# Optimization experiments

Hardware: AMD Instinct MI355X
Metric: run time of the kernel (lower is better)

The kernel has to match this reference:

```python
import jax, jax.numpy as jnp
import numpy as np

DIM = 4096
N_HEADS = 32
N_KV_HEADS = 8
HEAD_DIM = DIM // N_HEADS  # 128
SEQLEN = 2048
BATCH = 2
ROPE_THETA = 10000.0


def _precompute_freqs(seqlen, head_dim, theta):
    # matches torchtitan precompute_freqs_cis: freqs over even indices
    freqs = 1.0 / (theta ** (np.arange(0, head_dim, 2)[: head_dim // 2].astype(np.float32) / head_dim))
    t = np.arange(seqlen, dtype=np.float32)
    ang = np.outer(t, freqs)  # (S, head_dim//2)
    return jnp.asarray(np.cos(ang)), jnp.asarray(np.sin(ang))


def setup_inputs() -> dict:
    key = jax.random.key(0)
    kx, kq, kk, kv, ko = jax.random.split(key, 5)
    x = jax.random.normal(kx, (BATCH, SEQLEN, DIM), dtype=jnp.float32)
    wq = jax.random.normal(kq, (N_HEADS * HEAD_DIM, DIM), dtype=jnp.float32) * 0.02
    wk = jax.random.normal(kk, (N_KV_HEADS * HEAD_DIM, DIM), dtype=jnp.float32) * 0.02
    wv = jax.random.normal(kv, (N_KV_HEADS * HEAD_DIM, DIM), dtype=jnp.float32) * 0.02
    wo = jax.random.normal(ko, (DIM, N_HEADS * HEAD_DIM), dtype=jnp.float32) * 0.02
    cos, sin = _precompute_freqs(SEQLEN, HEAD_DIM, ROPE_THETA)
    return {"x": x, "cos": cos, "sin": sin, "wq": wq, "wk": wk, "wv": wv, "wo": wo}


def _apply_rope(t, cos, sin):
    # t: (B, S, H, hd); pairs (t[...,2i], t[...,2i+1]) rotated by angle
    tr = t.reshape(*t.shape[:-1], -1, 2)
    a, b = tr[..., 0], tr[..., 1]
    c = cos[None, :, None, :]  # (1, S, 1, hd//2)
    s = sin[None, :, None, :]
    out = jnp.stack([a * c - b * s, a * s + b * c], axis=-1)
    return out.reshape(t.shape)


def reference(x, cos, sin, wq, wk, wv, wo):
    B, S, D = x.shape
    hd = 2 * cos.shape[-1]
    H = wq.shape[0] // hd
    KVH = wk.shape[0] // hd
    n_rep = H // KVH

    q = (x @ wq.T).reshape(B, S, H, hd)
    k = (x @ wk.T).reshape(B, S, KVH, hd)
    v = (x @ wv.T).reshape(B, S, KVH, hd)

    q = _apply_rope(q, cos, sin)
    k = _apply_rope(k, cos, sin)

    # GQA: repeat_interleave kv heads (kept implicit via reshape of q into groups)
    qg = q.reshape(B, S, KVH, n_rep, hd)
    scale = 1.0 / jnp.sqrt(jnp.asarray(hd, dtype=x.dtype))
    # scores: (B, KVH, n_rep, S_q, S_k)
    scores = jnp.einsum("bsgrd,btgd->bgrst", qg, k) * scale
    causal = jnp.tril(jnp.ones((S, S), dtype=bool))
    scores = jnp.where(causal[None, None, None], scores, jnp.asarray(-1e30, dtype=scores.dtype))
    probs = jax.nn.softmax(scores, axis=-1)
    out = jnp.einsum("bgrst,btgd->bsgrd", probs, v).reshape(B, S, H * hd)
    return out @ wo.T
```

## Files before the change

### kernel.cpp

```cpp
#include <hip/hip_runtime.h>
#include <hip/hip_bf16.h>
#include <stdint.h>

#define DIM    4096
#define NH     32
#define NKVH   8
#define HD     128
#define SEQ    2048
#define BATCH  2
#define MTOT   (BATCH*SEQ)
#define SCALE  0.08838834764831845f

typedef __bf16 bf16_t;
typedef __bf16 bf16x8 __attribute__((ext_vector_type(8)));
typedef float  f32x4  __attribute__((ext_vector_type(4)));

#define AS1 __attribute__((address_space(1)))
#define AS3 __attribute__((address_space(3)))

__device__ __forceinline__ void gload_lds16(const void* g, void* l) {
    __builtin_amdgcn_global_load_lds((const AS1 void*)g, (AS3 void*)l, 16, 0, 0);
}

__device__ __forceinline__ void fence_barrier() {
    asm volatile("" ::: "memory");
    __builtin_amdgcn_s_barrier();
    asm volatile("" ::: "memory");
}

__global__ __launch_bounds__(256)
void cvt_f32_bf16(const float* __restrict__ in, bf16_t* __restrict__ out, int n4) {
    for (int i = blockIdx.x * blockDim.x + threadIdx.x; i < n4;
         i += gridDim.x * blockDim.x) {
        float4 v = reinterpret_cast<const float4*>(in)[i];
        union { bf16_t b[4]; uint2 u; } t;
        t.b[0] = (bf16_t)v.x; t.b[1] = (bf16_t)v.y;
        t.b[2] = (bf16_t)v.z; t.b[3] = (bf16_t)v.w;
        reinterpret_cast<uint2*>(out)[i] = t.u;
    }
}

__global__ __launch_bounds__(256)
void cvt_weights(const float* __restrict__ wq, const float* __restrict__ wk,
                 const float* __restrict__ wv, const float* __restrict__ wo,
                 bf16_t* __restrict__ out) {
    const int n0 = DIM * DIM / 4;
    const int n1 = NKVH * HD * DIM / 4;
    const int n2 = NKVH * HD * DIM / 4;
    const int n3 = DIM * DIM / 4;
    const int ntot = n0 + n1 + n2 + n3;
    for (int i = blockIdx.x * blockDim.x + threadIdx.x; i < ntot;
         i += gridDim.x * blockDim.x) {
        const float* src;
        int k = i;
        if (k < n0) src = wq;
        else if ((k -= n0) < n1) src = wk;
        else if ((k -= n1) < n2) src = wv;
        else { k -= n2; src = wo; }
        float4 v = reinterpret_cast<const float4*>(src)[k];
        union { bf16_t b[4]; uint2 u; } t;
        t.b[0] = (bf16_t)v.x; t.b[1] = (bf16_t)v.y;
        t.b[2] = (bf16_t)v.z; t.b[3] = (bf16_t)v.w;
        reinterpret_cast<uint2*>(out)[i] = t.u;
    }
}


__device__ __forceinline__ void stage_half(const bf16_t* gbase, int kt, int h,
                                           bf16_t* ldsdst, int tid, int w) {
#pragma unroll
    for (int t2 = 0; t2 < 2; ++t2) {
        int s = t2 * 512 + tid;
        int r = s >> 3, c = s & 7;
        gload_lds16(gbase + (size_t)(h * 128 + r) * DIM + kt + ((c ^ (r & 7)) * 8),
                    ldsdst + (size_t)(t2 * 512 + w * 64) * 8);
    }
}

__device__ __forceinline__ void read_a4(bf16x8 a[4][2], const bf16_t* Ahalf,
                                        int mh, int lr, int lg) {
#pragma unroll
    for (int mi = 0; mi < 4; ++mi) {
        int r = mh * 64 + mi * 16 + lr;
#pragma unroll
        for (int kk = 0; kk < 2; ++kk)
            a[mi][kk] = *(const bf16x8*)(Ahalf + r * 64 + ((kk * 4 + lg) ^ (r & 7)) * 8);
    }
}

__device__ __forceinline__ void read_b2(bf16x8 b[2][2], const bf16_t* Bhalf,
                                        int np, int rb, int lg) {
#pragma unroll
    for (int ni = 0; ni < 2; ++ni) {
        int r = rb + (np * 2 + ni) * 16;
#pragma unroll
        for (int kk = 0; kk < 2; ++kk)
            b[ni][kk] = *(const bf16x8*)(Bhalf + r * 64 + ((kk * 4 + lg) ^ (r & 7)) * 8);
    }
}

template<int MODE>
__global__ __launch_bounds__(512, 2)
void gemm8(const bf16_t* __restrict__ A,
           const bf16_t* __restrict__ B0,
           float* __restrict__ outF,
           bf16_t* __restrict__ outQ,
           bf16_t* __restrict__ outK,
           bf16_t* __restrict__ outV,
           const float* __restrict__ cosT,
           const float* __restrict__ sinT) {
    __shared__ __align__(16) bf16_t As[2][2][128 * 64];
    __shared__ __align__(16) bf16_t Bs[2][2][128 * 64];

    const int tid = threadIdx.x;
    const int l = tid & 63;
    const int w = tid >> 6;
    const int wm = w >> 2, wn = w & 3;
    const int lr = l & 15, lg = l >> 4;
    const int rb = (wn & 1) * 64 + lr;
    const int bh2 = wn >> 1;

    const int rowBase = blockIdx.x * 256;
    const int ct = blockIdx.y;

    const bf16_t* Ap = A + (size_t)rowBase * DIM;
    const bf16_t* Bp = B0 + (size_t)ct * 256 * DIM;

    f32x4 acc[8][4] = {};
    bf16x8 a0[4][2], a1[4][2];
    bf16x8 bA[2][2], bB[2][2];

    const int NT = DIM / 64;

    stage_half(Bp, 0,  0, &Bs[0][0][0], tid, w);
    stage_half(Bp, 0,  1, &Bs[0][1][0], tid, w);
    stage_half(Ap, 0,  0, &As[0][0][0], tid, w);
    stage_half(Ap, 0,  1, &As[0][1][0], tid, w);
    stage_half(Bp, 64, 0, &Bs[1][0][0], tid, w);
    stage_half(Bp, 64, 1, &Bs[1][1][0], tid, w);
    asm volatile("s_waitcnt vmcnt(4)" ::: "memory");
    fence_barrier();
    read_a4(a0, &As[0][wm][0], 0, lr, lg);
    read_b2(bA, &Bs[0][bh2][0], 0, rb, lg);

    for (int j = 0; j < NT; ++j) {
        const int s = j & 1;
        const bf16_t* Ah = &As[s][wm][0];
        const bf16_t* Bh = &Bs[s][bh2][0];
        const int ktA = ((j + 1 < NT) ? j + 1 : NT - 1) * 64;
        const int ktB = ((j + 2 < NT) ? j + 2 : NT - 1) * 64;

        read_b2(bB, Bh, 1, rb, lg);
        stage_half(Ap, ktA, 0, &As[s ^ 1][0][0], tid, w);
        asm volatile("s_waitcnt lgkmcnt(4)" ::: "memory");
        __builtin_amdgcn_s_setprio(1);
#pragma unroll
        for (int kk = 0; kk < 2; ++kk)
#pragma unroll
            for (int mi = 0; mi < 4; ++mi) {
                acc[mi][0] = __builtin_amdgcn_mfma_f32_16x16x32_bf16(a0[mi][kk], bA[0][kk], acc[mi][0], 0, 0, 0);
                acc[mi][1] = __builtin_amdgcn_mfma_f32_16x16x32_bf16(a0[mi][kk], bA[1][kk], acc[mi][1], 0, 0, 0);
            }
        __builtin_amdgcn_s_setprio(0);
        fence_barrier();

        read_a4(a1, Ah, 1, lr, lg);
        stage_half(Ap, ktA, 1, &As[s ^ 1][1][0], tid, w);
        asm volatile("s_waitcnt lgkmcnt(8)" ::: "memory");
        __builtin_amdgcn_s_setprio(1);
#pragma unroll
        for (int kk = 0; kk < 2; ++kk)
#pragma unroll
            for (int mi = 0; mi < 4; ++mi) {
                acc[mi][2] = __builtin_amdgcn_mfma_f32_16x16x32_bf16(a0[mi][kk], bB[0][kk], acc[mi][2], 0, 0, 0);
                acc[mi][3] = __builtin_amdgcn_mfma_f32_16x16x32_bf16(a0[mi][kk], bB[1][kk], acc[mi][3], 0, 0, 0);
            }
        __builtin_amdgcn_s_setprio(0);
        fence_barrier();

        stage_half(Bp, ktB, 0, &Bs[s][0][0], tid, w);
        asm volatile("s_waitcnt lgkmcnt(0)" ::: "memory");
        __builtin_amdgcn_s_setprio(1);
#pragma unroll
        for (int kk = 0; kk < 2; ++kk)
#pragma unroll
            for (int mi = 0; mi < 4; ++mi) {
                acc[mi + 4][0] = __builtin_amdgcn_mfma_f32_16x16x32_bf16(a1[mi][kk], bA[0][kk], acc[mi + 4][0], 0, 0, 0);
                acc[mi + 4][1] = __builtin_amdgcn_mfma_f32_16x16x32_bf16(a1[mi][kk], bA[1][kk], acc[mi + 4][1], 0, 0, 0);
            }
        __builtin_amdgcn_s_setprio(0);
        fence_barrier();

        stage_half(Bp, ktB, 1, &Bs[s][1][0], tid, w);
        __builtin_amdgcn_s_setprio(1);
#pragma unroll
        for (int kk = 0; kk < 2; ++kk)
#pragma unroll
            for (int mi = 0; mi < 4; ++mi) {
                acc[mi + 4][2] = __builtin_amdgcn_mfma_f32_16x16x32_bf16(a1[mi][kk], bB[0][kk], acc[mi + 4][2], 0, 0, 0);
                acc[mi + 4][3] = __builtin_amdgcn_mfma_f32_16x16x32_bf16(a1[mi][kk], bB[1][kk], acc[mi + 4][3], 0, 0, 0);
            }
        __builtin_amdgcn_s_setprio(0);
        asm volatile("s_waitcnt vmcnt(4)" ::: "memory");
        fence_barrier();
        if (j + 1 < NT) {
            read_a4(a0, &As[s ^ 1][wm][0], 0, lr, lg);
            read_b2(bA, &Bs[s ^ 1][bh2][0], 0, rb, lg);
        }
    }

#pragma unroll
    for (int mi = 0; mi < 8; ++mi) {
        int gmBase = rowBase + wm * 128 + mi * 16 + lg * 4;
#pragma unroll
        for (int ni = 0; ni < 4; ++ni) {
            f32x4 v4 = acc[mi][ni];
            int gn = ct * 256 + wn * 64 + ni * 16 + lr;
            if (MODE == 0) {
#pragma unroll
                for (int i = 0; i < 4; ++i)
                    outF[(size_t)(gmBase + i) * DIM + gn] = v4[i];
            } else {
                if (ct < 16) {
                    int h = gn >> 7, d = gn & 127, pi2 = d >> 1;
#pragma unroll
                    for (int i = 0; i < 4; ++i) {
                        float v = v4[i];
                        float pvv = __shfl_xor(v, 1);
                        int gm = gmBase + i;
                        int bb = gm >> 11, sidx = gm & (SEQ - 1);
                        float c = cosT[sidx * 64 + pi2], sn = sinT[sidx * 64 + pi2];
                        float o = (d & 1) ? (pvv * sn + v * c) : (v * c - pvv * sn);
                        outQ[((size_t)(bb * NH + h) * SEQ + sidx) * HD + d] = (bf16_t)o;
                    }
                } else if (ct < 20) {
                    int kn = gn - 4096;
                    int h = kn >> 7, d = kn & 127, pi2 = d >> 1;
#pragma unroll
                    for (int i = 0; i < 4; ++i) {
                        float v = v4[i];
                        float pvv = __shfl_xor(v, 1);
                        int gm = gmBase + i;
                        int bb = gm >> 11, sidx = gm & (SEQ - 1);
                        float c = cosT[sidx * 64 + pi2], sn = sinT[sidx * 64 + pi2];
                        float o = (d & 1) ? (pvv * sn + v * c) : (v * c - pvv * sn);
                        outK[((size_t)(bb * NKVH + h) * SEQ + sidx) * HD + d] = (bf16_t)o;
                    }
                } else {
                    int vn = gn - 5120;
                    int kvh = vn >> 7, d = vn & 127;
#pragma unroll
                    for (int i = 0; i < 4; ++i) {
                        float dummy = __shfl_xor(v4[i], 1); (void)dummy;
                        int gm = gmBase + i;
                        int bb = gm >> 11, sidx = gm & (SEQ - 1);
                        outV[((size_t)(bb * NKVH + kvh) * HD + d) * SEQ + sidx] = (bf16_t)v4[i];
                    }
                }
            }
        }
    }
}

__global__ __launch_bounds__(256, 2)
void attn_fwd(const bf16_t* __restrict__ Qr,
              const bf16_t* __restrict__ Kr,
              const bf16_t* __restrict__ Vt,
              bf16_t* __restrict__ Ob) {
    __shared__ __align__(16) bf16_t Ks[2][64 * 128];
    __shared__ __align__(16) bf16_t Vs[2][128 * 64];
    __shared__ __align__(16) bf16_t Ps[4][32 * 64];

    const int tid = threadIdx.x;
    const int l  = tid & 63;
    const int w  = tid >> 6;
    const int lr = l & 15, lg = l >> 4;
    const int e  = lr & 7;

    const int qt  = 15 - (blockIdx.x >> 6);
    const int bh  = blockIdx.x & 63;
    const int b   = bh >> 5;
    const int h   = bh & 31;
    const int kvh = h >> 2;
    const int q0  = qt * 128;
    const int nt  = 2 * qt + 2;
    const int qmin = q0 + w * 32;

    const bf16_t* kbase = Kr + (size_t)(b * NKVH + kvh) * SEQ * HD;
    const bf16_t* vbase = Vt + (size_t)(b * NKVH + kvh) * HD * SEQ;

    bf16x8 qf[2][4];
    const bf16_t* qp = Qr + ((size_t)(b * NH + h) * SEQ + qmin + lr) * HD;
#pragma unroll
    for (int mi = 0; mi < 2; ++mi)
#pragma unroll
        for (int kk = 0; kk < 4; ++kk)
            qf[mi][kk] = *(const bf16x8*)(qp + (size_t)mi * 16 * HD + kk * 32 + lg * 8);

    f32x4 oacc[2][8] = {};
    float mrow[2] = {-1e30f, -1e30f};
    float lsum[2] = {0.f, 0.f};

#pragma unroll
    for (int t2 = 0; t2 < 4; ++t2) {
        int s = t2 * 256 + tid;
        { int r = s >> 4, g = (s & 15) ^ (r & 7);
          gload_lds16(kbase + (size_t)r * HD + g * 8,
                      &Ks[0][(size_t)(t2 * 256 + w * 64) * 8]); }
        { int r = s >> 3, g = (s & 7) ^ (r & 7);
          gload_lds16(vbase + (size_t)r * SEQ + g * 8,
                      &Vs[0][(size_t)(t2 * 256 + w * 64) * 8]); }
    }
    __syncthreads();

    int cur = 0;
    for (int t = 0; t < nt; ++t) {
        if (t + 1 < nt) {
            const int kv1 = (t + 1) * 64;
#pragma unroll
            for (int t2 = 0; t2 < 4; ++t2) {
                int s = t2 * 256 + tid;
                { int r = s >> 4, g = (s & 15) ^ (r & 7);
                  gload_lds16(kbase + (size_t)(kv1 + r) * HD + g * 8,
                              &Ks[cur ^ 1][(size_t)(t2 * 256 + w * 64) * 8]); }
                { int r = s >> 3, g = (s & 7) ^ (r & 7);
                  gload_lds16(vbase + (size_t)r * SEQ + kv1 + g * 8,
                              &Vs[cur ^ 1][(size_t)(t2 * 256 + w * 64) * 8]); }
            }
        }

        const bool active = (t * 64) <= (qmin + 31);
        if (active) {
            const bool needMask = (t * 64 + 63) > qmin;

            f32x4 sf[2][4] = {};
#pragma unroll
            for (int kk = 0; kk < 4; ++kk)
#pragma unroll
                for (int nf = 0; nf < 4; ++nf) {
                    bf16x8 kf = *(const bf16x8*)(
                        &Ks[cur][(nf * 16 + lr) * 128 + ((kk * 4 + lg) ^ e) * 8]);
#pragma unroll
                    for (int mi = 0; mi < 2; ++mi)
                        sf[mi][nf] = __builtin_amdgcn_mfma_f32_16x16x32_bf16(
                            kf, qf[mi][kk], sf[mi][nf], 0, 0, 0);
                }

            float aO[2][4];
#pragma unroll
            for (int mi = 0; mi < 2; ++mi) {
                const int qrow = qmin + mi * 16 + lr;
                float mt = -1e30f;
#pragma unroll
                for (int nf = 0; nf < 4; ++nf)
#pragma unroll
                    for (int i = 0; i < 4; ++i) {
                        float sc = sf[mi][nf][i] * SCALE;
                        if (needMask && (t * 64 + nf * 16 + lg * 4 + i) > qrow)
                            sc = -1e30f;
                        sf[mi][nf][i] = sc;
                        mt = fmaxf(mt, sc);
                    }
                mt = fmaxf(mt, __shfl_xor(mt, 16));
                mt = fmaxf(mt, __shfl_xor(mt, 32));
                float mnew = fmaxf(mrow[mi], mt);
                float alpha = __expf(mrow[mi] - mnew);
                mrow[mi] = mnew;
                float rs = 0.f;
#pragma unroll
                for (int nf = 0; nf < 4; ++nf)
#pragma unroll
                    for (int i = 0; i < 4; ++i) {
                        float p = __expf(sf[mi][nf][i] - mnew);
                        sf[mi][nf][i] = p;
                        rs += p;
                    }
                rs += __shfl_xor(rs, 16);
                rs += __shfl_xor(rs, 32);
                lsum[mi] = lsum[mi] * alpha + rs;
#pragma unroll
                for (int i = 0; i < 4; ++i)
                    aO[mi][i] = __shfl(alpha, lg * 4 + i);
            }

#pragma unroll
            for (int mi = 0; mi < 2; ++mi)
#pragma unroll
                for (int df = 0; df < 8; ++df)
#pragma unroll
                    for (int i = 0; i < 4; ++i)
                        oacc[mi][df][i] *= aO[mi][i];

#pragma unroll
            for (int mi = 0; mi < 2; ++mi)
#pragma unroll
                for (int nf = 0; nf < 4; ++nf) {
                    union { bf16_t bb[4]; uint2 u; } pk;
#pragma unroll
                    for (int i = 0; i < 4; ++i) pk.bb[i] = (bf16_t)sf[mi][nf][i];
                    int addr = (mi * 16 + lr) * 64 +
                               (((nf * 2 + (lg >> 1)) ^ e) << 3) + (lg & 1) * 4;
                    *(uint2*)(&Ps[w][addr]) = pk.u;
                }
            asm volatile("s_waitcnt lgkmcnt(0)" ::: "memory");
            __builtin_amdgcn_sched_barrier(0);

            bf16x8 pf[2][2];
#pragma unroll
            for (int mi = 0; mi < 2; ++mi)
#pragma unroll
                for (int k2 = 0; k2 < 2; ++k2)
                    pf[mi][k2] = *(const bf16x8*)(
                        &Ps[w][(mi * 16 + lr) * 64 + ((k2 * 4 + lg) ^ e) * 8]);
#pragma unroll
            for (int df = 0; df < 8; ++df)
#pragma unroll
                for (int k2 = 0; k2 < 2; ++k2) {
                    bf16x8 vf = *(const bf16x8*)(
                        &Vs[cur][(df * 16 + lr) * 64 + ((k2 * 4 + lg) ^ e) * 8]);
#pragma unroll
                    for (int mi = 0; mi < 2; ++mi)
                        oacc[mi][df] = __builtin_amdgcn_mfma_f32_16x16x32_bf16(
                            pf[mi][k2], vf, oacc[mi][df], 0, 0, 0);
                }
        }
        __syncthreads();
        cur ^= 1;
    }

#pragma unroll
    for (int mi = 0; mi < 2; ++mi) {
        float ls[4];
#pragma unroll
        for (int i = 0; i < 4; ++i)
            ls[i] = 1.f / __shfl(lsum[mi], lg * 4 + i);
#pragma unroll
        for (int df = 0; df < 8; ++df)
#pragma unroll
            for (int i = 0; i < 4; ++i) {
                float o = oacc[mi][df][i] * ls[i];
                int gm = b * SEQ + qmin + mi * 16 + lg * 4 + i;
                int gn = h * HD + df * 16 + lr;
                Ob[(size_t)gm * DIM + gn] = (bf16_t)o;
            }
    }
}

extern "C" void kernel_launch(void* const* d_in, const int* in_sizes, int n_in,
                              void* d_out, int out_size, void* d_ws, size_t ws_size,
                              hipStream_t stream) {
    const float* x    = (const float*)d_in[0];
    const float* cosT = (const float*)d_in[1];
    const float* sinT = (const float*)d_in[2];
    const float* wq   = (const float*)d_in[3];
    const float* wk   = (const float*)d_in[4];
    const float* wv   = (const float*)d_in[5];
    const float* wo   = (const float*)d_in[6];

    bf16_t* p = (bf16_t*)d_ws;
    bf16_t* xb  = p; p += (size_t)MTOT * DIM;
    bf16_t* wb  = p; p += (size_t)(DIM + 2 * NKVH * HD + DIM) * DIM;
    bf16_t* Qr  = p; p += (size_t)MTOT * DIM;
    bf16_t* Kr  = p; p += (size_t)BATCH * NKVH * SEQ * HD;
    bf16_t* Vt  = p; p += (size_t)BATCH * NKVH * HD * SEQ;
    bf16_t* Ob  = p; p += (size_t)MTOT * DIM;

    bf16_t* wob = wb + (size_t)(DIM + 2 * NKVH * HD) * DIM;

    cvt_f32_bf16<<<2048, 256, 0, stream>>>(x, xb, MTOT * DIM / 4);
    cvt_weights<<<2048, 256, 0, stream>>>(wq, wk, wv, wo, wb);

    gemm8<3><<<dim3(16, 24), 512, 0, stream>>>(
        xb, wb, nullptr, Qr, Kr, Vt, cosT, sinT);

    attn_fwd<<<1024, 256, 0, stream>>>(Qr, Kr, Vt, Ob);

    gemm8<0><<<dim3(16, 16), 512, 0, stream>>>(
        Ob, wob, (float*)d_out, nullptr, nullptr, nullptr, nullptr, nullptr);
}
```

Before: 517.0 us.

## Fuse conversion kernels, reschedule GEMM pipeline, add lazy softmax rescaling

The x and weight fp32-to-bf16 conversions are merged into one launch writing a contiguous buffer, since xb and wb are adjacent in the workspace. The GEMM main loop is re-staged: fragments are read from LDS at the start of each quarter-step, and the global-to-LDS prefetch slots for A and B halves are reordered with adjusted vmcnt waits. The attention kernel skips the running-max update and output rescale when every lane's new max exceeds the old by at most 8, which saves the exp and oacc multiplies but lets exponentials grow up to e^8 before normalization. The extra barriers and full lgkmcnt(0) waits in the GEMM may reduce overlap.

```diff
diff --git a/kernel.cpp b/kernel.cpp
--- a/kernel.cpp
+++ b/kernel.cpp
@@ -29,31 +29,22 @@
 }
 
 __global__ __launch_bounds__(256)
-void cvt_f32_bf16(const float* __restrict__ in, bf16_t* __restrict__ out, int n4) {
-    for (int i = blockIdx.x * blockDim.x + threadIdx.x; i < n4;
-         i += gridDim.x * blockDim.x) {
-        float4 v = reinterpret_cast<const float4*>(in)[i];
-        union { bf16_t b[4]; uint2 u; } t;
-        t.b[0] = (bf16_t)v.x; t.b[1] = (bf16_t)v.y;
-        t.b[2] = (bf16_t)v.z; t.b[3] = (bf16_t)v.w;
-        reinterpret_cast<uint2*>(out)[i] = t.u;
-    }
-}
-
-__global__ __launch_bounds__(256)
-void cvt_weights(const float* __restrict__ wq, const float* __restrict__ wk,
-                 const float* __restrict__ wv, const float* __restrict__ wo,
-                 bf16_t* __restrict__ out) {
+void cvt_all(const float* __restrict__ x,
+             const float* __restrict__ wq, const float* __restrict__ wk,
+             const float* __restrict__ wv, const float* __restrict__ wo,
+             bf16_t* __restrict__ out) {
+    const int nx = MTOT * DIM / 4;
     const int n0 = DIM * DIM / 4;
     const int n1 = NKVH * HD * DIM / 4;
     const int n2 = NKVH * HD * DIM / 4;
     const int n3 = DIM * DIM / 4;
-    const int ntot = n0 + n1 + n2 + n3;
+    const int ntot = nx + n0 + n1 + n2 + n3;
     for (int i = blockIdx.x * blockDim.x + threadIdx.x; i < ntot;
          i += gridDim.x * blockDim.x) {
         const float* src;
         int k = i;
-        if (k < n0) src = wq;
+        if (k < nx) src = x;
+        else if ((k -= nx) < n0) src = wq;
         else if ((k -= n0) < n1) src = wk;
         else if ((k -= n1) < n2) src = wv;
         else { k -= n2; src = wo; }
@@ -101,14 +92,14 @@
 
 template<int MODE>
 __global__ __launch_bounds__(512, 2)
-void gemm8(const bf16_t* __restrict__ A,
-           const bf16_t* __restrict__ B0,
-           float* __restrict__ outF,
-           bf16_t* __restrict__ outQ,
-           bf16_t* __restrict__ outK,
-           bf16_t* __restrict__ outV,
-           const float* __restrict__ cosT,
-           const float* __restrict__ sinT) {
+void gemm8p(const bf16_t* __restrict__ A,
+            const bf16_t* __restrict__ B0,
+            float* __restrict__ outF,
+            bf16_t* __restrict__ outQ,
+            bf16_t* __restrict__ outK,
+            bf16_t* __restrict__ outV,
+            const float* __restrict__ cosT,
+            const float* __restrict__ sinT) {
     __shared__ __align__(16) bf16_t As[2][2][128 * 64];
     __shared__ __align__(16) bf16_t Bs[2][2][128 * 64];
 
@@ -127,86 +118,86 @@
     const bf16_t* Bp = B0 + (size_t)ct * 256 * DIM;
 
     f32x4 acc[8][4] = {};
-    bf16x8 a0[4][2], a1[4][2];
-    bf16x8 bA[2][2], bB[2][2];
+    bf16x8 a0[4][2], a1[4][2], b0[2][2], b1[2][2];
 
     const int NT = DIM / 64;
 
+    stage_half(Ap, 0,  0, &As[0][0][0], tid, w);
+    stage_half(Ap, 0,  1, &As[0][1][0], tid, w);
     stage_half(Bp, 0,  0, &Bs[0][0][0], tid, w);
     stage_half(Bp, 0,  1, &Bs[0][1][0], tid, w);
-    stage_half(Ap, 0,  0, &As[0][0][0], tid, w);
-    stage_half(Ap, 0,  1, &As[0][1][0], tid, w);
     stage_half(Bp, 64, 0, &Bs[1][0][0], tid, w);
     stage_half(Bp, 64, 1, &Bs[1][1][0], tid, w);
-    asm volatile("s_waitcnt vmcnt(4)" ::: "memory");
+    stage_half(Ap, 64, 0, &As[1][0][0], tid, w);
+    asm volatile("s_waitcnt vmcnt(6)" ::: "memory");
     fence_barrier();
-    read_a4(a0, &As[0][wm][0], 0, lr, lg);
-    read_b2(bA, &Bs[0][bh2][0], 0, rb, lg);
-
-    for (int j = 0; j < NT; ++j) {
-        const int s = j & 1;
+
+    for (int t = 0; t < NT; ++t) {
+        const int s = t & 1;
         const bf16_t* Ah = &As[s][wm][0];
         const bf16_t* Bh = &Bs[s][bh2][0];
-        const int ktA = ((j + 1 < NT) ? j + 1 : NT - 1) * 64;
-        const int ktB = ((j + 2 < NT) ? j + 2 : NT - 1) * 64;
-
-        read_b2(bB, Bh, 1, rb, lg);
-        stage_half(Ap, ktA, 0, &As[s ^ 1][0][0], tid, w);
-        asm volatile("s_waitcnt lgkmcnt(4)" ::: "memory");
-        __builtin_amdgcn_s_setprio(1);
-#pragma unroll
-        for (int kk = 0; kk < 2; ++kk)
-#pragma unroll
-            for (int mi = 0; mi < 4; ++mi) {
-                acc[mi][0] = __builtin_amdgcn_mfma_f32_16x16x32_bf16(a0[mi][kk], bA[0][kk], acc[mi][0], 0, 0, 0);
-                acc[mi][1] = __builtin_amdgcn_mfma_f32_16x16x32_bf16(a0[mi][kk], bA[1][kk], acc[mi][1], 0, 0, 0);
-            }
-        __builtin_amdgcn_s_setprio(0);
-        fence_barrier();
-
-        read_a4(a1, Ah, 1, lr, lg);
-        stage_half(Ap, ktA, 1, &As[s ^ 1][1][0], tid, w);
+        const int kt1 = ((t + 1 < NT) ? t + 1 : NT - 1) * 64;
+        const int kt2 = ((t + 2 < NT) ? t + 2 : NT - 1) * 64;
+
+        read_a4(a0, Ah, 0, lr, lg);
+        read_b2(b0, Bh, 0, rb, lg);
+        stage_half(Ap, kt1, 1, &As[s ^ 1][1][0], tid, w);
         asm volatile("s_waitcnt lgkmcnt(8)" ::: "memory");
-        __builtin_amdgcn_s_setprio(1);
-#pragma unroll
-        for (int kk = 0; kk < 2; ++kk)
-#pragma unroll
-            for (int mi = 0; mi < 4; ++mi) {
-                acc[mi][2] = __builtin_amdgcn_mfma_f32_16x16x32_bf16(a0[mi][kk], bB[0][kk], acc[mi][2], 0, 0, 0);
-                acc[mi][3] = __builtin_amdgcn_mfma_f32_16x16x32_bf16(a0[mi][kk], bB[1][kk], acc[mi][3], 0, 0, 0);
-            }
-        __builtin_amdgcn_s_setprio(0);
-        fence_barrier();
-
-        stage_half(Bp, ktB, 0, &Bs[s][0][0], tid, w);
+        fence_barrier();
         asm volatile("s_waitcnt lgkmcnt(0)" ::: "memory");
         __builtin_amdgcn_s_setprio(1);
 #pragma unroll
         for (int kk = 0; kk < 2; ++kk)
 #pragma unroll
             for (int mi = 0; mi < 4; ++mi) {
-                acc[mi + 4][0] = __builtin_amdgcn_mfma_f32_16x16x32_bf16(a1[mi][kk], bA[0][kk], acc[mi + 4][0], 0, 0, 0);
-                acc[mi + 4][1] = __builtin_amdgcn_mfma_f32_16x16x32_bf16(a1[mi][kk], bA[1][kk], acc[mi + 4][1], 0, 0, 0);
+                acc[mi][0] = __builtin_amdgcn_mfma_f32_16x16x32_bf16(a0[mi][kk], b0[0][kk], acc[mi][0], 0, 0, 0);
+                acc[mi][1] = __builtin_amdgcn_mfma_f32_16x16x32_bf16(a0[mi][kk], b0[1][kk], acc[mi][1], 0, 0, 0);
             }
         __builtin_amdgcn_s_setprio(0);
         fence_barrier();
 
-        stage_half(Bp, ktB, 1, &Bs[s][1][0], tid, w);
+        read_b2(b1, Bh, 1, rb, lg);
+        fence_barrier();
+        asm volatile("s_waitcnt lgkmcnt(0)" ::: "memory");
         __builtin_amdgcn_s_setprio(1);
 #pragma unroll
         for (int kk = 0; kk < 2; ++kk)
 #pragma unroll
             for (int mi = 0; mi < 4; ++mi) {
-                acc[mi + 4][2] = __builtin_amdgcn_mfma_f32_16x16x32_bf16(a1[mi][kk], bB[0][kk], acc[mi + 4][2], 0, 0, 0);
-                acc[mi + 4][3] = __builtin_amdgcn_mfma_f32_16x16x32_bf16(a1[mi][kk], bB[1][kk], acc[mi + 4][3], 0, 0, 0);
+                acc[mi][2] = __builtin_amdgcn_mfma_f32_16x16x32_bf16(a0[mi][kk], b1[0][kk], acc[mi][2], 0, 0, 0);
+                acc[mi][3] = __builtin_amdgcn_mfma_f32_16x16x32_bf16(a0[mi][kk], b1[1][kk], acc[mi][3], 0, 0, 0);
             }
         __builtin_amdgcn_s_setprio(0);
-        asm volatile("s_waitcnt vmcnt(4)" ::: "memory");
-        fence_barrier();
-        if (j + 1 < NT) {
-            read_a4(a0, &As[s ^ 1][wm][0], 0, lr, lg);
-            read_b2(bA, &Bs[s ^ 1][bh2][0], 0, rb, lg);
-        }
+        fence_barrier();
+
+        read_a4(a1, Ah, 1, lr, lg);
+        stage_half(Bp, kt2, 0, &Bs[s][0][0], tid, w);
+        fence_barrier();
+        asm volatile("s_waitcnt lgkmcnt(0)" ::: "memory");
+        __builtin_amdgcn_s_setprio(1);
+#pragma unroll
+        for (int kk = 0; kk < 2; ++kk)
+#pragma unroll
+            for (int mi = 0; mi < 4; ++mi) {
+                acc[mi + 4][0] = __builtin_amdgcn_mfma_f32_16x16x32_bf16(a1[mi][kk], b0[0][kk], acc[mi + 4][0], 0, 0, 0);
+                acc[mi + 4][1] = __builtin_amdgcn_mfma_f32_16x16x32_bf16(a1[mi][kk], b0[1][kk], acc[mi + 4][1], 0, 0, 0);
+            }
+        __builtin_amdgcn_s_setprio(0);
+        fence_barrier();
+
+        stage_half(Bp, kt2, 1, &Bs[s][1][0], tid, w);
+        stage_half(Ap, kt2, 0, &As[s][0][0], tid, w);
+        __builtin_amdgcn_s_setprio(1);
+#pragma unroll
+        for (int kk = 0; kk < 2; ++kk)
+#pragma unroll
+            for (int mi = 0; mi < 4; ++mi) {
+                acc[mi + 4][2] = __builtin_amdgcn_mfma_f32_16x16x32_bf16(a1[mi][kk], b1[0][kk], acc[mi + 4][2], 0, 0, 0);
+                acc[mi + 4][3] = __builtin_amdgcn_mfma_f32_16x16x32_bf16(a1[mi][kk], b1[1][kk], acc[mi + 4][3], 0, 0, 0);
+            }
+        __builtin_amdgcn_s_setprio(0);
+        asm volatile("s_waitcnt vmcnt(6)" ::: "memory");
+        fence_barrier();
     }
 
 #pragma unroll
@@ -221,7 +212,7 @@
                 for (int i = 0; i < 4; ++i)
                     outF[(size_t)(gmBase + i) * DIM + gn] = v4[i];
             } else {
-                if (ct < 16) {
+                if (gn < 4096) {
                     int h = gn >> 7, d = gn & 127, pi2 = d >> 1;
 #pragma unroll
                     for (int i = 0; i < 4; ++i) {
@@ -233,7 +224,7 @@
                         float o = (d & 1) ? (pvv * sn + v * c) : (v * c - pvv * sn);
                         outQ[((size_t)(bb * NH + h) * SEQ + sidx) * HD + d] = (bf16_t)o;
                     }
-                } else if (ct < 20) {
+                } else if (gn < 5120) {
                     int kn = gn - 4096;
                     int h = kn >> 7, d = kn & 127, pi2 = d >> 1;
 #pragma unroll
@@ -346,7 +337,6 @@
                             kf, qf[mi][kk], sf[mi][nf], 0, 0, 0);
                 }
 
-            float aO[2][4];
 #pragma unroll
             for (int mi = 0; mi < 2; ++mi) {
                 const int qrow = qmin + mi * 16 + lr;
@@ -363,9 +353,10 @@
                     }
                 mt = fmaxf(mt, __shfl_xor(mt, 16));
                 mt = fmaxf(mt, __shfl_xor(mt, 32));
-                float mnew = fmaxf(mrow[mi], mt);
-                float alpha = __expf(mrow[mi] - mnew);
-                mrow[mi] = mnew;
+
+                const bool skip = __all(mt - mrow[mi] <= 8.0f);
+                const float mnew = skip ? mrow[mi] : fmaxf(mrow[mi], mt);
+
                 float rs = 0.f;
 #pragma unroll
                 for (int nf = 0; nf < 4; ++nf)
@@ -377,19 +368,24 @@
                     }
                 rs += __shfl_xor(rs, 16);
                 rs += __shfl_xor(rs, 32);
-                lsum[mi] = lsum[mi] * alpha + rs;
-#pragma unroll
-                for (int i = 0; i < 4; ++i)
-                    aO[mi][i] = __shfl(alpha, lg * 4 + i);
-            }
-
-#pragma unroll
-            for (int mi = 0; mi < 2; ++mi)
-#pragma unroll
-                for (int df = 0; df < 8; ++df)
+
+                if (skip) {
+                    lsum[mi] += rs;
+                } else {
+                    float alpha = __expf(mrow[mi] - mnew);
+                    mrow[mi] = mnew;
+                    lsum[mi] = lsum[mi] * alpha + rs;
+                    float aO[4];
 #pragma unroll
                     for (int i = 0; i < 4; ++i)
-                        oacc[mi][df][i] *= aO[mi][i];
+                        aO[i] = __shfl(alpha, lg * 4 + i);
+#pragma unroll
+                    for (int df = 0; df < 8; ++df)
+#pragma unroll
+                        for (int i = 0; i < 4; ++i)
+                            oacc[mi][df][i] *= aO[i];
+                }
+            }
 
 #pragma unroll
             for (int mi = 0; mi < 2; ++mi)
@@ -467,14 +463,13 @@
 
     bf16_t* wob = wb + (size_t)(DIM + 2 * NKVH * HD) * DIM;
 
-    cvt_f32_bf16<<<2048, 256, 0, stream>>>(x, xb, MTOT * DIM / 4);
-    cvt_weights<<<2048, 256, 0, stream>>>(wq, wk, wv, wo, wb);
-
-    gemm8<3><<<dim3(16, 24), 512, 0, stream>>>(
+    cvt_all<<<2048, 256, 0, stream>>>(x, wq, wk, wv, wo, xb);
+
+    gemm8p<3><<<dim3(16, 24), 512, 0, stream>>>(
         xb, wb, nullptr, Qr, Kr, Vt, cosT, sinT);
 
     attn_fwd<<<1024, 256, 0, stream>>>(Qr, Kr, Vt, Ob);
 
-    gemm8<0><<<dim3(16, 16), 512, 0, stream>>>(
+    gemm8p<0><<<dim3(16, 16), 512, 0, stream>>>(
         Ob, wob, (float*)d_out, nullptr, nullptr, nullptr, nullptr, nullptr);
 }
```

Result: slower. 583.6 us (+12.9%).
